# Optimization experiments

Measured on AMD Instinct MI355X. Metric: run time of the kernel, lower is better.

Reference implementation:

```python
import jax, jax.numpy as jnp
import numpy as np

EPS = 1e-10


def _log_scaling(feats):
    """Raw feats (..., 15): xmin,ymin,xmax,ymax,area,angle,pca_big,pca_small,hu1..hu7
    -> (..., 17): xmin..area, log|pca_big..hu7|, lshape, cosangle, sinangle."""
    lshape = jnp.sqrt(feats[..., 7:8]) / (jnp.sqrt(feats[..., 6:7]) + EPS)
    cosangle = jnp.cos(feats[..., 5:6])
    sinangle = jnp.sin(feats[..., 5:6])
    logged = jnp.log(jnp.abs(feats[..., 5:]) + EPS)  # cols 5..14 logged
    # original drops the (logged) angle column 5 and keeps logged cols 6..14
    return jnp.concatenate([feats[..., :5], logged[..., 1:], lshape, cosangle, sinangle], axis=-1)


def _make_parents(n_trees, P, seed=0):
    """Valid topologically-ordered tree: parent[p] < p, parent[0] = 0 (root)."""
    rng = np.random.default_rng(seed)
    idx = np.arange(P)
    high = np.maximum(idx, 1)
    par = rng.integers(0, 2**31 - 1, size=(n_trees, P)) % high[None, :]
    par[:, 0] = 0
    return par.astype(np.int32)


def setup_inputs() -> dict:
    key = jax.random.key(0)
    k1, k2, k3, k4 = jax.random.split(key, 4)
    B, N, H, W = 2, 2, 1024, 1024
    P = H * W
    x = jax.random.normal(k1, (B, N, H, W), dtype=jnp.float32) * 10.0
    weight = jax.random.uniform(k2, (N, 17, 1), dtype=jnp.float32, minval=-0.01, maxval=0.01)
    bias = jnp.zeros((N, 1), dtype=jnp.float32)
    attrs = jax.random.uniform(k3, (B, N, P, 15), dtype=jnp.float32) * 4.0
    parents = jnp.asarray(_make_parents(B * N, P).reshape(B, N, P))
    return {"x": x, "weight": weight, "bias": bias, "attrs": attrs, "parents": parents}


def _path_sum(contrib_pad, par_pad, P):
    """Pointer-doubling root-to-node path sums over a tree with sentinel at index P."""
    iters = max(int(np.ceil(np.log2(max(P, 2)))), 1)

    def body(i, carry):
        v, p = carry
        return v + v[p], p[p]

    v, _ = jax.lax.fori_loop(0, iters, body, (contrib_pad, par_pad))
    return v[:P]


def reference(x, weight, bias, attrs, parents):
    B, N, H, W = x.shape
    P = H * W
    xf = x.reshape(B, N, P)
    idx = jnp.arange(P, dtype=parents.dtype)
    is_root = parents == idx  # (B,N,P)
    parent_vals = jnp.take_along_axis(xf, parents, axis=-1)
    diff = jnp.where(is_root, xf, xf - parent_vals)  # per-node gray-level increment
    feats = _log_scaling(attrs)  # (B,N,P,17)
    lin = jnp.einsum('bnpf,nfo->bnpo', feats, weight) + bias[None, :, None, :]
    scores = jax.nn.sigmoid(lin[..., 0])  # (B,N,P)
    contrib = diff * scores
    # sentinel node P with contribution 0; roots point at the sentinel
    sent = jnp.full((B, N, 1), P, dtype=parents.dtype)
    par_pad = jnp.concatenate([jnp.where(is_root, P, parents), sent], axis=-1)
    contrib_pad = jnp.concatenate([contrib, jnp.zeros((B, N, 1), x.dtype)], axis=-1)
    out = jax.vmap(jax.vmap(lambda c, p: _path_sum(c, p, P)))(contrib_pad, par_pad)
    return out.reshape(B, N, H, W)
```

## Files before the change

### kernel.cpp

```cpp
#include <hip/hip_runtime.h>
#include <math.h>

#define EPSF 1e-10f
#define P_NODES (1 << 20)
#define T_FRONT 65536

struct __align__(8) NodePair {
    float v;
    int   par;
};

__global__ __launch_bounds__(256) void score_kernel(
    const float* __restrict__ x,
    const float* __restrict__ weight,
    const float* __restrict__ bias,
    const float* __restrict__ attrs,
    const int*   __restrict__ parents,
    NodePair*    __restrict__ dst,
    int N)
{
    __shared__ float sA[256 * 15];

    const int t = threadIdx.x;
    const int blockBase = blockIdx.x * 256;
    const int idx = blockBase + t;

    const float* ab = attrs + (size_t)blockBase * 15;
#pragma unroll
    for (int j = 0; j < 15; ++j)
        sA[j * 256 + t] = ab[j * 256 + t];

    const int tree = blockBase >> 20;
    const int n    = tree % N;
    const float* w = weight + n * 17;
    const float  b = bias[n];

    __syncthreads();

    const float* a = &sA[t * 15];

    float acc = b;
    acc += a[0] * w[0];
    acc += a[1] * w[1];
    acc += a[2] * w[2];
    acc += a[3] * w[3];
    acc += a[4] * w[4];

    const float a5 = a[5];
    const float a6 = a[6];
    const float a7 = a[7];

    acc += __logf(fabsf(a6)    + EPSF) * w[5];
    acc += __logf(fabsf(a7)    + EPSF) * w[6];
    acc += __logf(fabsf(a[8])  + EPSF) * w[7];
    acc += __logf(fabsf(a[9])  + EPSF) * w[8];
    acc += __logf(fabsf(a[10]) + EPSF) * w[9];
    acc += __logf(fabsf(a[11]) + EPSF) * w[10];
    acc += __logf(fabsf(a[12]) + EPSF) * w[11];
    acc += __logf(fabsf(a[13]) + EPSF) * w[12];
    acc += __logf(fabsf(a[14]) + EPSF) * w[13];

    const float lshape = __fsqrt_rn(a7) / (__fsqrt_rn(a6) + EPSF);
    acc += lshape * w[14];
    acc += __cosf(a5) * w[15];
    acc += __sinf(a5) * w[16];

    const float score = 1.0f / (1.0f + __expf(-acc));

    const int   p   = idx & (P_NODES - 1);
    const int   par = parents[idx];
    const float xv  = x[idx];

    NodePair r;
    if (par == p) {
        r.v   = xv * score;
        r.par = -1;
    } else {
        r.v   = (xv - x[(idx - p) + par]) * score;
        r.par = par;
    }
    dst[idx] = r;
}

__global__ __launch_bounds__(256) void frontier_kernel(
    const NodePair* __restrict__ pairs,
    float*          __restrict__ S,
    int nTrees)
{
    const int i = blockIdx.x * blockDim.x + threadIdx.x;
    if (i >= nTrees * T_FRONT) return;

    const int tree = i / T_FRONT;
    const int p    = i - tree * T_FRONT;
    const int base = tree << 20;

    NodePair r = pairs[base + p];
    float s = r.v;
    int   c = r.par;
    while (c >= 0) {
        NodePair q = pairs[base + c];
        s += q.v;
        c  = q.par;
    }
    S[i] = s;
}

__global__ __launch_bounds__(256) void resolve_kernel(
    const NodePair* __restrict__ pairs,
    const float*    __restrict__ S,
    float*          __restrict__ out,
    int nHalf)
{
    const int i = blockIdx.x * blockDim.x + threadIdx.x;
    if (i >= nHalf) return;

    const int idx0 = i * 2;
    const int base = idx0 & ~(P_NODES - 1);
    const int tree = idx0 >> 20;
    const float* St = S + (size_t)tree * T_FRONT;

    float4 r = ((const float4*)pairs)[i];
    float s0 = r.x;  int c0 = __float_as_int(r.y);
    float s1 = r.z;  int c1 = __float_as_int(r.w);

    bool a0 = (c0 >= T_FRONT);
    bool a1 = (c1 >= T_FRONT);
    while (a0 || a1) {
        NodePair q0, q1;
        if (a0) q0 = pairs[base + c0];
        if (a1) q1 = pairs[base + c1];
        if (a0) { s0 += q0.v; c0 = q0.par; a0 = (c0 >= T_FRONT); }
        if (a1) { s1 += q1.v; c1 = q1.par; a1 = (c1 >= T_FRONT); }
    }
    if (c0 >= 0) s0 += St[c0];
    if (c1 >= 0) s1 += St[c1];

    float2 o; o.x = s0; o.y = s1;
    ((float2*)out)[i] = o;
}

extern "C" void kernel_launch(void* const* d_in, const int* in_sizes, int n_in,
                              void* d_out, int out_size, void* d_ws, size_t ws_size,
                              hipStream_t stream)
{
    const float* x       = (const float*)d_in[0];
    const float* weight  = (const float*)d_in[1];
    const float* bias    = (const float*)d_in[2];
    const float* attrs   = (const float*)d_in[3];
    const int*   parents = (const int*)d_in[4];
    float*       out     = (float*)d_out;

    const int total  = in_sizes[0];
    const int N      = in_sizes[1] / 17;
    const int nTrees = total >> 20;

    NodePair* pairs = (NodePair*)d_ws;
    float*    S     = (float*)((char*)d_ws + (size_t)total * sizeof(NodePair));

    const int block = 256;
    const int grid  = (total + block - 1) / block;
    const int nHalf = total / 2;
    const int gridH = (nHalf + block - 1) / block;
    const int nF    = nTrees * T_FRONT;
    const int gridF = (nF + block - 1) / block;

    score_kernel<<<grid, block, 0, stream>>>(x, weight, bias, attrs, parents,
                                             pairs, N);
    frontier_kernel<<<gridF, block, 0, stream>>>(pairs, S, nTrees);
    resolve_kernel<<<gridH, block, 0, stream>>>(pairs, S, out, nHalf);
}
```

Before: 440.6 us.

## Resolve path sums in three frontier levels writing directly into output

Replaces the two-stage frontier/resolve scheme with three stages: the first 64K nodes walk fully to the root, then nodes in [64K,256K) walk only until they reach a node below 64K and add its finished sum from out, then the remaining nodes do the same against the 256K prefix. This shortens the pointer chases in the large final stage and removes the separate S buffer. The attrs staging load in the score kernel is also vectorised to float4. The cost is an extra kernel launch and a serial dependency between the stages.

```diff
diff --git a/kernel.cpp b/kernel.cpp
--- a/kernel.cpp
+++ b/kernel.cpp
@@ -4,6 +4,7 @@
 #define EPSF 1e-10f
 #define P_NODES (1 << 20)
 #define T_FRONT 65536
+#define T_MID   262144
 
 struct __align__(8) NodePair {
     float v;
@@ -25,10 +26,11 @@
     const int blockBase = blockIdx.x * 256;
     const int idx = blockBase + t;
 
-    const float* ab = attrs + (size_t)blockBase * 15;
+    const float4* ab4 = (const float4*)(attrs + (size_t)blockBase * 15);
+    float4* sA4 = (float4*)sA;
 #pragma unroll
-    for (int j = 0; j < 15; ++j)
-        sA[j * 256 + t] = ab[j * 256 + t];
+    for (int k = t; k < 960; k += 256)
+        sA4[k] = ab4[k];
 
     const int tree = blockBase >> 20;
     const int n    = tree % N;
@@ -84,59 +86,61 @@
 
 __global__ __launch_bounds__(256) void frontier_kernel(
     const NodePair* __restrict__ pairs,
-    float*          __restrict__ S,
-    int nTrees)
+    float*          __restrict__ out)
 {
-    const int i = blockIdx.x * blockDim.x + threadIdx.x;
-    if (i >= nTrees * T_FRONT) return;
+    const int j  = blockIdx.x * blockDim.x + threadIdx.x;
+    const int p0 = j * 2;
+    if (p0 >= T_FRONT) return;
 
-    const int tree = i / T_FRONT;
-    const int p    = i - tree * T_FRONT;
-    const int base = tree << 20;
+    const int base = blockIdx.y << 20;
+    const NodePair* tp = pairs + base;
 
-    NodePair r = pairs[base + p];
-    float s = r.v;
-    int   c = r.par;
-    while (c >= 0) {
-        NodePair q = pairs[base + c];
-        s += q.v;
-        c  = q.par;
-    }
-    S[i] = s;
-}
-
-__global__ __launch_bounds__(256) void resolve_kernel(
-    const NodePair* __restrict__ pairs,
-    const float*    __restrict__ S,
-    float*          __restrict__ out,
-    int nHalf)
-{
-    const int i = blockIdx.x * blockDim.x + threadIdx.x;
-    if (i >= nHalf) return;
-
-    const int idx0 = i * 2;
-    const int base = idx0 & ~(P_NODES - 1);
-    const int tree = idx0 >> 20;
-    const float* St = S + (size_t)tree * T_FRONT;
-
-    float4 r = ((const float4*)pairs)[i];
+    float4 r = *(const float4*)(tp + p0);
     float s0 = r.x;  int c0 = __float_as_int(r.y);
     float s1 = r.z;  int c1 = __float_as_int(r.w);
 
-    bool a0 = (c0 >= T_FRONT);
-    bool a1 = (c1 >= T_FRONT);
+    while (c0 >= 0 || c1 >= 0) {
+        NodePair q0, q1;
+        bool a0 = (c0 >= 0), a1 = (c1 >= 0);
+        if (a0) q0 = tp[c0];
+        if (a1) q1 = tp[c1];
+        if (a0) { s0 += q0.v; c0 = q0.par; }
+        if (a1) { s1 += q1.v; c1 = q1.par; }
+    }
+
+    float2 o; o.x = s0; o.y = s1;
+    *(float2*)(out + base + p0) = o;
+}
+
+__global__ __launch_bounds__(256) void chunk_kernel(
+    const NodePair* __restrict__ pairs,
+    float*          __restrict__ out,
+    int lo, int hi)
+{
+    const int j  = blockIdx.x * blockDim.x + threadIdx.x;
+    const int p0 = lo + j * 2;
+    if (p0 >= hi) return;
+
+    const int base = blockIdx.y << 20;
+    const NodePair* tp = pairs + base;
+
+    float4 r = *(const float4*)(tp + p0);
+    float s0 = r.x;  int c0 = __float_as_int(r.y);
+    float s1 = r.z;  int c1 = __float_as_int(r.w);
+
+    bool a0 = (c0 >= lo), a1 = (c1 >= lo);
     while (a0 || a1) {
         NodePair q0, q1;
-        if (a0) q0 = pairs[base + c0];
-        if (a1) q1 = pairs[base + c1];
-        if (a0) { s0 += q0.v; c0 = q0.par; a0 = (c0 >= T_FRONT); }
-        if (a1) { s1 += q1.v; c1 = q1.par; a1 = (c1 >= T_FRONT); }
+        if (a0) q0 = tp[c0];
+        if (a1) q1 = tp[c1];
+        if (a0) { s0 += q0.v; c0 = q0.par; a0 = (c0 >= lo); }
+        if (a1) { s1 += q1.v; c1 = q1.par; a1 = (c1 >= lo); }
     }
-    if (c0 >= 0) s0 += St[c0];
-    if (c1 >= 0) s1 += St[c1];
+    s0 += out[base + c0];
+    s1 += out[base + c1];
 
     float2 o; o.x = s0; o.y = s1;
-    ((float2*)out)[i] = o;
+    *(float2*)(out + base + p0) = o;
 }
 
 extern "C" void kernel_launch(void* const* d_in, const int* in_sizes, int n_in,
@@ -155,17 +159,23 @@
     const int nTrees = total >> 20;
 
     NodePair* pairs = (NodePair*)d_ws;
-    float*    S     = (float*)((char*)d_ws + (size_t)total * sizeof(NodePair));
 
     const int block = 256;
     const int grid  = (total + block - 1) / block;
-    const int nHalf = total / 2;
-    const int gridH = (nHalf + block - 1) / block;
-    const int nF    = nTrees * T_FRONT;
-    const int gridF = (nF + block - 1) / block;
 
     score_kernel<<<grid, block, 0, stream>>>(x, weight, bias, attrs, parents,
                                              pairs, N);
-    frontier_kernel<<<gridF, block, 0, stream>>>(pairs, S, nTrees);
-    resolve_kernel<<<gridH, block, 0, stream>>>(pairs, S, out, nHalf);
+
+    {
+        dim3 g((T_FRONT / 2 + block - 1) / block, nTrees);
+        frontier_kernel<<<g, block, 0, stream>>>(pairs, out);
+    }
+    {
+        dim3 g(((T_MID - T_FRONT) / 2 + block - 1) / block, nTrees);
+        chunk_kernel<<<g, block, 0, stream>>>(pairs, out, T_FRONT, T_MID);
+    }
+    {
+        dim3 g(((P_NODES - T_MID) / 2 + block - 1) / block, nTrees);
+        chunk_kernel<<<g, block, 0, stream>>>(pairs, out, T_MID, P_NODES);
+    }
 }
```

After: 438.6 us. About the same (-0.4%).
